# Kernel optimization log

Measured on AMD Instinct MI355X. Metric: run time of the kernel, lower is better.

The kernel has to match this reference:

```python
import jax, jax.numpy as jnp
import numpy as np

B, N, K = 8, 2048, 30  # graphs, points per graph, kNN neighbors


def setup_inputs() -> dict:
    key = jax.random.key(0)
    ks = jax.random.split(key, 16)
    w = lambda k, s: jax.random.normal(k, s, jnp.float32) * 0.05
    z = lambda s: jnp.zeros(s, jnp.float32)
    return {
        "x": jax.random.normal(ks[0], (B * N, 3), jnp.float32),
        "pos": jax.random.normal(ks[1], (B * N, 3), jnp.float32),
        "w1a": w(ks[2], (12, 64)), "b1a": z(64),
        "w1b": w(ks[3], (64, 64)), "b1b": z(64),
        "w2a": w(ks[4], (128, 64)), "b2a": z(64),
        "w2b": w(ks[5], (64, 64)), "b2b": z(64),
        "w3a": w(ks[6], (128, 64)), "b3a": z(64),
        "w3b": w(ks[7], (64, 64)), "b3b": z(64),
        "hw1": w(ks[8], (192, 1024)), "hb1": z(1024),
        "hw2": w(ks[9], (1024, 512)), "hb2": z(512),
        "hw3": w(ks[10], (512, 128)), "hb3": z(128),
        "batch": jnp.repeat(jnp.arange(B, dtype=jnp.int32), N),
        "batch_size": B,
    }


def _knn_idx(f):
    # f: [B,N,d] -> indices of K nearest neighbors (incl. self), [B,N,K]
    d2 = jnp.sum(f * f, axis=-1)  # [B,N]
    dist = d2[:, :, None] + d2[:, None, :] - 2.0 * jnp.einsum('bnd,bmd->bnm', f, f)
    return jax.lax.top_k(-dist, K)[1]


def _edge_conv(f, wa, ba, wb, bb):
    # DynamicEdgeConv: kNN graph on f, message MLP([x_i, x_j - x_i]), max-aggregate
    idx = _knn_idx(f)                                   # [B,N,K]
    xj = jax.vmap(lambda ff, ii: ff[ii])(f, idx)        # [B,N,K,d]
    xi = f[:, :, None, :]
    e = jnp.concatenate([jnp.broadcast_to(xi, xj.shape), xj - xi], axis=-1)
    h = jax.nn.relu(e @ wa + ba)                        # MLP layer 1 (act)
    h = h @ wb + bb                                     # MLP layer 2 (plain last)
    return jnp.max(h, axis=2)                           # max aggr -> [B,N,64]


def reference(x, pos, w1a, b1a, w1b, b1b, w2a, b2a, w2b, b2b, w3a, b3a, w3b, b3b,
              hw1, hb1, hw2, hb2, hw3, hb3, batch, batch_size):
    x0 = jnp.concatenate([x, pos], axis=-1).reshape(batch_size, -1, 6)  # [B,N,6]
    x1 = _edge_conv(x0, w1a, b1a, w1b, b1b)
    x2 = _edge_conv(x1, w2a, b2a, w2b, b2b)
    x3 = _edge_conv(x2, w3a, b3a, w3b, b3b)
    feat = jnp.concatenate([x1, x2, x3], axis=-1)       # [B,N,192]
    h = jax.nn.relu(feat @ hw1 + hb1)                   # head MLP (dropout=eval)
    h = jax.nn.relu(h @ hw2 + hb2)
    out = h @ hw3 + hb3                                 # [B,N,out_channels]
    return out
```

## Files before the change

kernel.cpp:

```cpp
#include <hip/hip_runtime.h>
#include <math.h>

#define BATCH 8
#define NPER 2048
#define NPTS (BATCH*NPER)
#define KNN 30

typedef __attribute__((ext_vector_type(8))) short bf16x8;
typedef __attribute__((ext_vector_type(4))) float f32x4;

__device__ __forceinline__ ushort f2bf(float x) {
    unsigned u = __float_as_uint(x);
    unsigned r = (u + 0x7fffu + ((u >> 16) & 1u)) >> 16;
    return (ushort)r;
}
__device__ __forceinline__ float bf2f(ushort h) {
    return __uint_as_float(((unsigned)h) << 16);
}

__global__ void concat_kernel(const float* __restrict__ x, const float* __restrict__ pos,
                              float* __restrict__ x0) {
    int n = blockIdx.x * blockDim.x + threadIdx.x;
    if (n >= NPTS) return;
#pragma unroll
    for (int d = 0; d < 3; ++d) {
        x0[n*6 + d]     = x[n*3 + d];
        x0[n*6 + 3 + d] = pos[n*3 + d];
    }
}

template<int D>
__global__ void d2_kernel(const float* __restrict__ f, int stride, float* __restrict__ d2) {
    int n = blockIdx.x * blockDim.x + threadIdx.x;
    if (n >= NPTS) return;
    const float* r = f + (size_t)n * stride;
    float s = 0.f;
#pragma unroll
    for (int d = 0; d < D; ++d) s += r[d]*r[d];
    d2[n] = s;
}

template<int D>
__global__ __launch_bounds__(256, 4) void knn4_kernel(const float* __restrict__ f, int stride,
                                                      const float* __restrict__ d2,
                                                      int* __restrict__ idx) {
    __shared__ float sdist[4][NPER];
    __shared__ float sxi[4][(D+3)/4*4];
    __shared__ float sd2n[4];
    int t = threadIdx.x;
    int n0 = blockIdx.x * 4;
    int base = (n0 >> 11) << 11;

    if (t < 4*D) {
        int q = t / D, d = t - q*D;
        sxi[q][d] = f[(size_t)(n0 + q)*stride + d];
    }
    if (t < 4) sd2n[t] = d2[n0 + t];
    __syncthreads();

#pragma unroll 1
    for (int j = 0; j < NPER/256; ++j) {
        int ml = t + 256*j;
        int m = base + ml;
        const float* fm = f + (size_t)m*stride;
        float d2m = d2[m];
        float dot0 = 0.f, dot1 = 0.f, dot2 = 0.f, dot3 = 0.f;
#pragma unroll
        for (int d = 0; d < D; ++d) {
            float a = fm[d];
            dot0 += a*sxi[0][d];
            dot1 += a*sxi[1][d];
            dot2 += a*sxi[2][d];
            dot3 += a*sxi[3][d];
        }
        sdist[0][ml] = sd2n[0] + d2m - 2.f*dot0;
        sdist[1][ml] = sd2n[1] + d2m - 2.f*dot1;
        sdist[2][ml] = sd2n[2] + d2m - 2.f*dot2;
        sdist[3][ml] = sd2n[3] + d2m - 2.f*dot3;
    }
    __syncthreads();

    int w = t >> 6, lane = t & 63;
    int n = n0 + w;

    unsigned u[NPER/64];
#pragma unroll
    for (int i = 0; i < NPER/64; ++i) {
        float dv = sdist[w][lane + 64*i];
        int b = __float_as_int(dv);
        u[i] = (unsigned)(b ^ ((b >> 31) | 0x80000000));
    }

    unsigned T = 0u;
#pragma unroll
    for (int bit = 31; bit >= 0; --bit) {
        unsigned C = T | (1u << bit);
        int c = 0;
#pragma unroll
        for (int i = 0; i < NPER/64; ++i) c += (u[i] < C) ? 1 : 0;
#pragma unroll
        for (int off = 1; off < 64; off <<= 1) c += __shfl_xor(c, off);
        if (c < KNN) T = C;
    }

    unsigned lm = 0u, em = 0u;
#pragma unroll
    for (int i = 0; i < NPER/64; ++i) {
        lm |= (u[i] < T)  ? (1u << i) : 0u;
        em |= (u[i] == T) ? (1u << i) : 0u;
    }
    int nl = __popc(lm);
    int inc = nl;
#pragma unroll
    for (int off = 1; off < 64; off <<= 1) {
        int y = __shfl_up(inc, off);
        if (lane >= off) inc += y;
    }
    int excl = inc - nl;
    int total_less = __shfl(inc, 63);

    int* op = idx + (size_t)n * KNN;
    int slot = excl;
#pragma unroll
    for (int i = 0; i < NPER/64; ++i) {
        if (lm & (1u << i)) { op[slot] = base + i*64 + lane; ++slot; }
    }

    int need = KNN - total_less;
    int running = 0;
#pragma unroll
    for (int i = 0; i < NPER/64; ++i) {
        unsigned long long bal = __ballot((em >> i) & 1u);
        if (bal) {
            unsigned long long lt = bal & ((1ull << lane) - 1ull);
            int r = running + __popcll(lt);
            if (((em >> i) & 1u) && r < need) op[total_less + r] = base + i*64 + lane;
            running += (int)__popcll(bal);
        }
    }
}

__global__ __launch_bounds__(256) void transpose64_kernel(const float* __restrict__ fin, int stride,
                                                          float* __restrict__ fT) {
    __shared__ float tile[64][65];
    int t = threadIdx.x;
    int n0 = blockIdx.x * 64;
#pragma unroll
    for (int i = 0; i < 4; ++i) {
        int id = t + 256*i;
        int r = id >> 4, c4 = (id & 15) * 4;
        float4 v = *reinterpret_cast<const float4*>(&fin[(size_t)(n0 + r)*stride + c4]);
        tile[r][c4] = v.x; tile[r][c4+1] = v.y; tile[r][c4+2] = v.z; tile[r][c4+3] = v.w;
    }
    __syncthreads();
#pragma unroll
    for (int i = 0; i < 16; ++i) {
        int id = t + 256*i;
        int d = id >> 6, nn = id & 63;
        fT[(size_t)d * NPTS + n0 + nn] = tile[nn][d];
    }
}

__global__ __launch_bounds__(256) void knn6_kernel(const float* __restrict__ fq, int qstride,
                                                   const float* __restrict__ fT,
                                                   const float* __restrict__ d2,
                                                   int* __restrict__ idx) {
    __shared__ float sdist[4][NPER];
    __shared__ float sq[4][64];
    __shared__ float sd2n[4];
    int t = threadIdx.x;
    int n0 = blockIdx.x * 4;
    int base = (n0 >> 11) << 11;

    {
        int q = t >> 6, d = t & 63;
        sq[q][d] = fq[(size_t)(n0 + q)*qstride + d];
    }
    if (t < 4) sd2n[t] = d2[n0 + t];
    __syncthreads();

    float acc0[8], acc1[8], acc2[8], acc3[8];
#pragma unroll
    for (int j = 0; j < 8; ++j) { acc0[j] = 0.f; acc1[j] = 0.f; acc2[j] = 0.f; acc3[j] = 0.f; }

    int cbase = base + 8*t;

#pragma unroll 2
    for (int dc = 0; dc < 16; ++dc) {
        int d0 = dc * 4;
        float4 q0 = *reinterpret_cast<const float4*>(&sq[0][d0]);
        float4 q1 = *reinterpret_cast<const float4*>(&sq[1][d0]);
        float4 q2 = *reinterpret_cast<const float4*>(&sq[2][d0]);
        float4 q3 = *reinterpret_cast<const float4*>(&sq[3][d0]);
        float qa0[4] = {q0.x, q0.y, q0.z, q0.w};
        float qa1[4] = {q1.x, q1.y, q1.z, q1.w};
        float qa2[4] = {q2.x, q2.y, q2.z, q2.w};
        float qa3[4] = {q3.x, q3.y, q3.z, q3.w};
#pragma unroll
        for (int dd = 0; dd < 4; ++dd) {
            const float* cp = fT + (size_t)(d0 + dd) * NPTS + cbase;
            float4 c0 = *reinterpret_cast<const float4*>(cp);
            float4 c1 = *reinterpret_cast<const float4*>(cp + 4);
            float cv[8] = {c0.x,c0.y,c0.z,c0.w,c1.x,c1.y,c1.z,c1.w};
#pragma unroll
            for (int j = 0; j < 8; ++j) {
                acc0[j] += cv[j]*qa0[dd];
                acc1[j] += cv[j]*qa1[dd];
                acc2[j] += cv[j]*qa2[dd];
                acc3[j] += cv[j]*qa3[dd];
            }
        }
    }

    {
        float dn0 = sd2n[0], dn1 = sd2n[1], dn2 = sd2n[2], dn3 = sd2n[3];
        float4 dm0 = *reinterpret_cast<const float4*>(&d2[cbase]);
        float4 dm1 = *reinterpret_cast<const float4*>(&d2[cbase + 4]);
        float dmv[8] = {dm0.x,dm0.y,dm0.z,dm0.w,dm1.x,dm1.y,dm1.z,dm1.w};
#pragma unroll
        for (int j = 0; j < 8; ++j) {
            int ml = 8*t + j;
            sdist[0][ml] = dn0 + dmv[j] - 2.f*acc0[j];
            sdist[1][ml] = dn1 + dmv[j] - 2.f*acc1[j];
            sdist[2][ml] = dn2 + dmv[j] - 2.f*acc2[j];
            sdist[3][ml] = dn3 + dmv[j] - 2.f*acc3[j];
        }
    }
    __syncthreads();

    int w = t >> 6, lane = t & 63;
    int n = n0 + w;

    unsigned u[NPER/64];
#pragma unroll
    for (int i = 0; i < NPER/64; ++i) {
        float dv = sdist[w][lane + 64*i];
        int b = __float_as_int(dv);
        u[i] = (unsigned)(b ^ ((b >> 31) | 0x80000000));
    }

    unsigned T = 0u;
#pragma unroll
    for (int bit = 31; bit >= 0; --bit) {
        unsigned C = T | (1u << bit);
        int c = 0;
#pragma unroll
        for (int i = 0; i < NPER/64; ++i) c += (u[i] < C) ? 1 : 0;
#pragma unroll
        for (int off = 1; off < 64; off <<= 1) c += __shfl_xor(c, off);
        if (c < KNN) T = C;
    }

    unsigned lm = 0u, em = 0u;
#pragma unroll
    for (int i = 0; i < NPER/64; ++i) {
        lm |= (u[i] < T)  ? (1u << i) : 0u;
        em |= (u[i] == T) ? (1u << i) : 0u;
    }
    int nl = __popc(lm);
    int inc = nl;
#pragma unroll
    for (int off = 1; off < 64; off <<= 1) {
        int y = __shfl_up(inc, off);
        if (lane >= off) inc += y;
    }
    int excl = inc - nl;
    int total_less = __shfl(inc, 63);

    int* op = idx + (size_t)n * KNN;
    int slot = excl;
#pragma unroll
    for (int i = 0; i < NPER/64; ++i) {
        if (lm & (1u << i)) { op[slot] = base + i*64 + lane; ++slot; }
    }

    int need = KNN - total_less;
    int running = 0;
#pragma unroll
    for (int i = 0; i < NPER/64; ++i) {
        unsigned long long bal = __ballot((em >> i) & 1u);
        if (bal) {
            unsigned long long lt = bal & ((1ull << lane) - 1ull);
            int r = running + __popcll(lt);
            if (((em >> i) & 1u) && r < need) op[total_less + r] = base + i*64 + lane;
            running += (int)__popcll(bal);
        }
    }
}

template<int D>
__global__ __launch_bounds__(256) void gmat_kernel(const float* __restrict__ fin, int in_stride,
                                                   const float* __restrict__ wa,
                                                   float* __restrict__ G) {
    constexpr int DP = (D+3)/4*4;
    __shared__ float sF[64][DP];
    int t = threadIdx.x;
    int row0 = blockIdx.x * 64;
    for (int i = t; i < 64*D; i += 256) {
        int r = i / D, c = i - r*D;
        sF[r][c] = fin[(size_t)(row0 + r)*in_stride + c];
    }
    int w = t >> 6, lane = t & 63;
    float wreg[D];
#pragma unroll
    for (int d = 0; d < D; ++d) wreg[d] = wa[(size_t)(D + d)*64 + lane];
    __syncthreads();
#pragma unroll 1
    for (int pi = 0; pi < 16; ++pi) {
        int p = w*16 + pi;
        float acc = 0.f;
        if constexpr (D % 4 == 0) {
#pragma unroll
            for (int d = 0; d < D; d += 4) {
                float4 fv = *reinterpret_cast<const float4*>(&sF[p][d]);
                acc += fv.x*wreg[d] + fv.y*wreg[d+1] + fv.z*wreg[d+2] + fv.w*wreg[d+3];
            }
        } else {
#pragma unroll
            for (int d = 0; d < D; ++d) acc += sF[p][d]*wreg[d];
        }
        G[(size_t)(row0 + p)*64 + lane] = acc;
    }
}

template<int D>
__global__ __launch_bounds__(256) void edgeconv2_kernel(const float* __restrict__ fin, int in_stride,
                                const float* __restrict__ G,
                                const int* __restrict__ idx,
                                const float* __restrict__ wa, const float* __restrict__ ba,
                                const float* __restrict__ wb, const float* __restrict__ bb,
                                float* __restrict__ fout, int out_stride) {
    __shared__ float sxi[4][(D+3)/4*4];
    __shared__ float sh1[4][2][64];
    int t = threadIdx.x;
    int w = t >> 6, lane = t & 63;
    int n = blockIdx.x * 4 + w;

    float wbc[64];
#pragma unroll
    for (int k = 0; k < 64; ++k) wbc[k] = wb[(size_t)k*64 + lane];
    float bbc = bb[lane];

    if (lane < D) sxi[w][lane] = fin[(size_t)n * in_stride + lane];
    __syncthreads();

    float basec = ba[lane];
#pragma unroll
    for (int d = 0; d < D; ++d)
        basec += sxi[w][d] * (wa[(size_t)d*64 + lane] - wa[(size_t)(D + d)*64 + lane]);

    const int* ip = idx + (size_t)n * KNN;
    int2 jp = *reinterpret_cast<const int2*>(ip);
    float g0 = G[(size_t)jp.x*64 + lane];
    float g1 = G[(size_t)jp.y*64 + lane];
    float maxv = -3.4e38f;
#pragma unroll 1
    for (int jj = 0; jj < KNN; jj += 2) {
        sh1[w][0][lane] = fmaxf(basec + g0, 0.f);
        sh1[w][1][lane] = fmaxf(basec + g1, 0.f);
        int2 jn;
        bool more = (jj + 2 < KNN);
        if (more) jn = *reinterpret_cast<const int2*>(ip + jj + 2);
        __syncthreads();
        if (more) {
            g0 = G[(size_t)jn.x*64 + lane];
            g1 = G[(size_t)jn.y*64 + lane];
        }
        float h20 = bbc, h21 = bbc;
#pragma unroll
        for (int k = 0; k < 64; k += 4) {
            float4 a = *reinterpret_cast<const float4*>(&sh1[w][0][k]);
            float4 b = *reinterpret_cast<const float4*>(&sh1[w][1][k]);
            h20 += a.x*wbc[k] + a.y*wbc[k+1] + a.z*wbc[k+2] + a.w*wbc[k+3];
            h21 += b.x*wbc[k] + b.y*wbc[k+1] + b.z*wbc[k+2] + b.w*wbc[k+3];
        }
        maxv = fmaxf(maxv, fmaxf(h20, h21));
        __syncthreads();
    }
    fout[(size_t)n * out_stride + lane] = maxv;
}

__global__ void wsplit_kernel(const float* __restrict__ w, int K, int N,
                              ushort* __restrict__ hi, ushort* __restrict__ lo, int total) {
    int i = blockIdx.x * 256 + threadIdx.x;
    if (i >= total) return;
    int n = i / K, k = i - n*K;
    float x = w[(size_t)k * N + n];
    ushort h = f2bf(x);
    hi[i] = h;
    lo[i] = f2bf(x - bf2f(h));
}

template<bool RELU>
__global__ __launch_bounds__(256) void mlp_gemm_kernel(
    const float* __restrict__ A, int lda, int K,
    const ushort* __restrict__ Bhi, const ushort* __restrict__ Blo,
    const float* __restrict__ bias, float* __restrict__ C, int N)
{
    __shared__ __align__(16) ushort sAh[64*40];
    __shared__ __align__(16) ushort sAl[64*40];
    __shared__ __align__(16) ushort sBh[64*40];
    __shared__ __align__(16) ushort sBl[64*40];
    int t = threadIdx.x;
    int row0 = blockIdx.x * 64;
    int n0   = blockIdx.y * 64;
    int r = t >> 2, sg = (t & 3) * 8;
    int lane = t & 63, w = t >> 6;
    int wr = w & 1, wc = w >> 1;
    int fr = lane & 15, fk = (lane >> 4) * 8;

    f32x4 acc00 = {0.f,0.f,0.f,0.f}, acc01 = {0.f,0.f,0.f,0.f};
    f32x4 acc10 = {0.f,0.f,0.f,0.f}, acc11 = {0.f,0.f,0.f,0.f};

    const int nk = K / 32;
#pragma unroll 1
    for (int kc = 0; kc < nk; ++kc) {
        int k0 = kc * 32;
        const float* ap = A + (size_t)(row0 + r) * lda + k0 + sg;
        float4 av0 = *reinterpret_cast<const float4*>(ap);
        float4 av1 = *reinterpret_cast<const float4*>(ap + 4);
        float av[8] = {av0.x,av0.y,av0.z,av0.w,av1.x,av1.y,av1.z,av1.w};
        uint ph[4], pl[4];
#pragma unroll
        for (int i = 0; i < 4; ++i) {
            ushort h0 = f2bf(av[2*i]);
            ushort l0 = f2bf(av[2*i]   - bf2f(h0));
            ushort h1 = f2bf(av[2*i+1]);
            ushort l1 = f2bf(av[2*i+1] - bf2f(h1));
            ph[i] = (uint)h0 | ((uint)h1 << 16);
            pl[i] = (uint)l0 | ((uint)l1 << 16);
        }
        uint4 bh = *reinterpret_cast<const uint4*>(Bhi + (size_t)(n0 + r) * K + k0 + sg);
        uint4 bl = *reinterpret_cast<const uint4*>(Blo + (size_t)(n0 + r) * K + k0 + sg);
        __syncthreads();
        *reinterpret_cast<uint4*>(&sAh[r*40 + sg]) = make_uint4(ph[0],ph[1],ph[2],ph[3]);
        *reinterpret_cast<uint4*>(&sAl[r*40 + sg]) = make_uint4(pl[0],pl[1],pl[2],pl[3]);
        *reinterpret_cast<uint4*>(&sBh[r*40 + sg]) = bh;
        *reinterpret_cast<uint4*>(&sBl[r*40 + sg]) = bl;
        __syncthreads();

        bf16x8 a0h = *reinterpret_cast<const bf16x8*>(&sAh[(wr*32 + fr)*40 + fk]);
        bf16x8 a1h = *reinterpret_cast<const bf16x8*>(&sAh[(wr*32 + 16 + fr)*40 + fk]);
        bf16x8 a0l = *reinterpret_cast<const bf16x8*>(&sAl[(wr*32 + fr)*40 + fk]);
        bf16x8 a1l = *reinterpret_cast<const bf16x8*>(&sAl[(wr*32 + 16 + fr)*40 + fk]);
        bf16x8 b0h = *reinterpret_cast<const bf16x8*>(&sBh[(wc*32 + fr)*40 + fk]);
        bf16x8 b1h = *reinterpret_cast<const bf16x8*>(&sBh[(wc*32 + 16 + fr)*40 + fk]);
        bf16x8 b0l = *reinterpret_cast<const bf16x8*>(&sBl[(wc*32 + fr)*40 + fk]);
        bf16x8 b1l = *reinterpret_cast<const bf16x8*>(&sBl[(wc*32 + 16 + fr)*40 + fk]);

        acc00 = __builtin_amdgcn_mfma_f32_16x16x32_bf16(a0h, b0h, acc00, 0, 0, 0);
        acc00 = __builtin_amdgcn_mfma_f32_16x16x32_bf16(a0h, b0l, acc00, 0, 0, 0);
        acc00 = __builtin_amdgcn_mfma_f32_16x16x32_bf16(a0l, b0h, acc00, 0, 0, 0);
        acc01 = __builtin_amdgcn_mfma_f32_16x16x32_bf16(a0h, b1h, acc01, 0, 0, 0);
        acc01 = __builtin_amdgcn_mfma_f32_16x16x32_bf16(a0h, b1l, acc01, 0, 0, 0);
        acc01 = __builtin_amdgcn_mfma_f32_16x16x32_bf16(a0l, b1h, acc01, 0, 0, 0);
        acc10 = __builtin_amdgcn_mfma_f32_16x16x32_bf16(a1h, b0h, acc10, 0, 0, 0);
        acc10 = __builtin_amdgcn_mfma_f32_16x16x32_bf16(a1h, b0l, acc10, 0, 0, 0);
        acc10 = __builtin_amdgcn_mfma_f32_16x16x32_bf16(a1l, b0h, acc10, 0, 0, 0);
        acc11 = __builtin_amdgcn_mfma_f32_16x16x32_bf16(a1h, b1h, acc11, 0, 0, 0);
        acc11 = __builtin_amdgcn_mfma_f32_16x16x32_bf16(a1h, b1l, acc11, 0, 0, 0);
        acc11 = __builtin_amdgcn_mfma_f32_16x16x32_bf16(a1l, b1h, acc11, 0, 0, 0);
    }

    int orow = row0 + wr*32 + (lane >> 4)*4;
    int ocol = n0 + wc*32 + fr;
    float bc0 = bias[ocol];
    float bc1 = bias[ocol + 16];
#pragma unroll
    for (int j = 0; j < 4; ++j) {
        float v00 = acc00[j] + bc0;
        float v01 = acc01[j] + bc1;
        float v10 = acc10[j] + bc0;
        float v11 = acc11[j] + bc1;
        if (RELU) {
            v00 = fmaxf(v00, 0.f); v01 = fmaxf(v01, 0.f);
            v10 = fmaxf(v10, 0.f); v11 = fmaxf(v11, 0.f);
        }
        C[(size_t)(orow + j)*N + ocol]           = v00;
        C[(size_t)(orow + j)*N + ocol + 16]      = v01;
        C[(size_t)(orow + 16 + j)*N + ocol]      = v10;
        C[(size_t)(orow + 16 + j)*N + ocol + 16] = v11;
    }
}

__global__ __launch_bounds__(256) void head_kernel(const float* __restrict__ feat,
                            const float* __restrict__ hw1, const float* __restrict__ hb1,
                            const float* __restrict__ hw2, const float* __restrict__ hb2,
                            const float* __restrict__ hw3, const float* __restrict__ hb3,
                            float* __restrict__ out) {
    __shared__ float smem[16384];
    float* sfeat = smem;
    float* sh1   = smem + 6144;
    int t = threadIdx.x;
    int row0 = blockIdx.x * 32;

    for (int i = t; i < 32*192; i += 256) sfeat[i] = feat[(size_t)row0*192 + i];
    __syncthreads();

    int c4 = t & 127, rh = t >> 7;
    float4 acc2[16];
    {
        float4 b = *reinterpret_cast<const float4*>(&hb2[4*c4]);
#pragma unroll
        for (int i = 0; i < 16; ++i) acc2[i] = b;
    }
    int c1 = t & 63, rg = t >> 6;

    for (int chunk = 0; chunk < 8; ++chunk) {
        int k0 = chunk * 128;
        float acc1a[8], acc1b[8];
        {
            float ba_ = hb1[k0 + c1], bb_ = hb1[k0 + 64 + c1];
#pragma unroll
            for (int i = 0; i < 8; ++i) { acc1a[i] = ba_; acc1b[i] = bb_; }
        }
#pragma unroll 1
        for (int k = 0; k < 192; k += 4) {
            float wA0 = hw1[(size_t)(k+0)*1024 + k0 + c1];
            float wA1 = hw1[(size_t)(k+1)*1024 + k0 + c1];
            float wA2 = hw1[(size_t)(k+2)*1024 + k0 + c1];
            float wA3 = hw1[(size_t)(k+3)*1024 + k0 + c1];
            float wB0 = hw1[(size_t)(k+0)*1024 + k0 + 64 + c1];
            float wB1 = hw1[(size_t)(k+1)*1024 + k0 + 64 + c1];
            float wB2 = hw1[(size_t)(k+2)*1024 + k0 + 64 + c1];
            float wB3 = hw1[(size_t)(k+3)*1024 + k0 + 64 + c1];
#pragma unroll
            for (int i = 0; i < 8; ++i) {
                float4 fv = *reinterpret_cast<const float4*>(&sfeat[(rg + 4*i)*192 + k]);
                acc1a[i] += fv.x*wA0 + fv.y*wA1 + fv.z*wA2 + fv.w*wA3;
                acc1b[i] += fv.x*wB0 + fv.y*wB1 + fv.z*wB2 + fv.w*wB3;
            }
        }
#pragma unroll
        for (int i = 0; i < 8; ++i) {
            sh1[(rg + 4*i)*128 + c1]      = fmaxf(acc1a[i], 0.f);
            sh1[(rg + 4*i)*128 + 64 + c1] = fmaxf(acc1b[i], 0.f);
        }
        __syncthreads();
        float4 wn[4];
#pragma unroll
        for (int q = 0; q < 4; ++q)
            wn[q] = *reinterpret_cast<const float4*>(&hw2[(size_t)(k0 + q)*512 + 4*c4]);
#pragma unroll 1
        for (int k = 0; k < 128; k += 4) {
            float4 wv[4];
#pragma unroll
            for (int q = 0; q < 4; ++q) wv[q] = wn[q];
            if (k + 4 < 128) {
#pragma unroll
                for (int q = 0; q < 4; ++q)
                    wn[q] = *reinterpret_cast<const float4*>(&hw2[(size_t)(k0 + k + 4 + q)*512 + 4*c4]);
            }
#pragma unroll
            for (int i = 0; i < 16; ++i) {
                float4 h4 = *reinterpret_cast<const float4*>(&sh1[(rh + 2*i)*128 + k]);
                acc2[i].x += h4.x*wv[0].x + h4.y*wv[1].x + h4.z*wv[2].x + h4.w*wv[3].x;
                acc2[i].y += h4.x*wv[0].y + h4.y*wv[1].y + h4.z*wv[2].y + h4.w*wv[3].y;
                acc2[i].z += h4.x*wv[0].z + h4.y*wv[1].z + h4.z*wv[2].z + h4.w*wv[3].z;
                acc2[i].w += h4.x*wv[0].w + h4.y*wv[1].w + h4.z*wv[2].w + h4.w*wv[3].w;
            }
        }
        __syncthreads();
    }
#pragma unroll
    for (int i = 0; i < 16; ++i) {
        float4 v;
        v.x = fmaxf(acc2[i].x, 0.f); v.y = fmaxf(acc2[i].y, 0.f);
        v.z = fmaxf(acc2[i].z, 0.f); v.w = fmaxf(acc2[i].w, 0.f);
        *reinterpret_cast<float4*>(&smem[(rh + 2*i)*512 + 4*c4]) = v;
    }
    __syncthreads();
    int c3 = t & 63, rg3 = t >> 6;
    float acc3a[8], acc3b[8];
    {
        float ba_ = hb3[c3], bb_ = hb3[c3 + 64];
#pragma unroll
        for (int i = 0; i < 8; ++i) { acc3a[i] = ba_; acc3b[i] = bb_; }
    }
#pragma unroll 1
    for (int k = 0; k < 512; k += 4) {
        float wA0 = hw3[(size_t)(k+0)*128 + c3];
        float wA1 = hw3[(size_t)(k+1)*128 + c3];
        float wA2 = hw3[(size_t)(k+2)*128 + c3];
        float wA3 = hw3[(size_t)(k+3)*128 + c3];
        float wB0 = hw3[(size_t)(k+0)*128 + c3 + 64];
        float wB1 = hw3[(size_t)(k+1)*128 + c3 + 64];
        float wB2 = hw3[(size_t)(k+2)*128 + c3 + 64];
        float wB3 = hw3[(size_t)(k+3)*128 + c3 + 64];
#pragma unroll
        for (int i = 0; i < 8; ++i) {
            float4 h4 = *reinterpret_cast<const float4*>(&smem[(rg3 + 4*i)*512 + k]);
            acc3a[i] += h4.x*wA0 + h4.y*wA1 + h4.z*wA2 + h4.w*wA3;
            acc3b[i] += h4.x*wB0 + h4.y*wB1 + h4.z*wB2 + h4.w*wB3;
        }
    }
#pragma unroll
    for (int i = 0; i < 8; ++i) {
        out[(size_t)(row0 + rg3 + 4*i)*128 + c3]      = acc3a[i];
        out[(size_t)(row0 + rg3 + 4*i)*128 + c3 + 64] = acc3b[i];
    }
}

extern "C" void kernel_launch(void* const* d_in, const int* in_sizes, int n_in,
                              void* d_out, int out_size, void* d_ws, size_t ws_size,
                              hipStream_t stream) {
    (void)in_sizes; (void)n_in; (void)out_size;
    const float* x   = (const float*)d_in[0];
    const float* pos = (const float*)d_in[1];
    const float* w1a = (const float*)d_in[2];
    const float* b1a = (const float*)d_in[3];
    const float* w1b = (const float*)d_in[4];
    const float* b1b = (const float*)d_in[5];
    const float* w2a = (const float*)d_in[6];
    const float* b2a = (const float*)d_in[7];
    const float* w2b = (const float*)d_in[8];
    const float* b2b = (const float*)d_in[9];
    const float* w3a = (const float*)d_in[10];
    const float* b3a = (const float*)d_in[11];
    const float* w3b = (const float*)d_in[12];
    const float* b3b = (const float*)d_in[13];
    const float* hw1 = (const float*)d_in[14];
    const float* hb1 = (const float*)d_in[15];
    const float* hw2 = (const float*)d_in[16];
    const float* hb2 = (const float*)d_in[17];
    const float* hw3 = (const float*)d_in[18];
    const float* hb3 = (const float*)d_in[19];
    float* out = (float*)d_out;

    float* ws = (float*)d_ws;
    float* x0   = ws;
    float* feat = ws + 98304;
    float* d2b  = ws + 3244032;
    int*   idxb = (int*)(ws + 3260416);
    float* G    = ws + 3751936;
    ushort* w1h = (ushort*)(ws + 4800512);
    ushort* w1l = (ushort*)(ws + 4898816);
    ushort* w2h = (ushort*)(ws + 4997120);
    ushort* w2l = (ushort*)(ws + 5259264);
    ushort* w3h = (ushort*)(ws + 5521408);
    ushort* w3l = (ushort*)(ws + 5554176);
    const size_t base_units = 5586944;

    float* fT = G;

    int ns = 0;
    {
        const int cands[5] = {1, 2, 4, 8, 16};
        for (int ci = 0; ci < 5; ++ci) {
            int c = cands[ci];
            size_t need = (base_units + (size_t)(NPTS / c) * 1536) * 4;
            if (need <= ws_size) { ns = c; break; }
        }
    }

    concat_kernel<<<NPTS/256, 256, 0, stream>>>(x, pos, x0);

    d2_kernel<6><<<NPTS/256, 256, 0, stream>>>(x0, 6, d2b);
    knn4_kernel<6><<<NPTS/4, 256, 0, stream>>>(x0, 6, d2b, idxb);
    gmat_kernel<6><<<NPTS/64, 256, 0, stream>>>(x0, 6, w1a, G);
    edgeconv2_kernel<6><<<NPTS/4, 256, 0, stream>>>(x0, 6, G, idxb, w1a, b1a, w1b, b1b, feat, 192);

    d2_kernel<64><<<NPTS/256, 256, 0, stream>>>(feat, 192, d2b);
    transpose64_kernel<<<NPTS/64, 256, 0, stream>>>(feat, 192, fT);
    knn6_kernel<<<NPTS/4, 256, 0, stream>>>(feat, 192, fT, d2b, idxb);
    gmat_kernel<64><<<NPTS/64, 256, 0, stream>>>(feat, 192, w2a, G);
    edgeconv2_kernel<64><<<NPTS/4, 256, 0, stream>>>(feat, 192, G, idxb, w2a, b2a, w2b, b2b, feat + 64, 192);

    d2_kernel<64><<<NPTS/256, 256, 0, stream>>>(feat + 64, 192, d2b);
    transpose64_kernel<<<NPTS/64, 256, 0, stream>>>(feat + 64, 192, fT);
    knn6_kernel<<<NPTS/4, 256, 0, stream>>>(feat + 64, 192, fT, d2b, idxb);
    gmat_kernel<64><<<NPTS/64, 256, 0, stream>>>(feat + 64, 192, w3a, G);
    edgeconv2_kernel<64><<<NPTS/4, 256, 0, stream>>>(feat + 64, 192, G, idxb, w3a, b3a, w3b, b3b, feat + 128, 192);

    if (ns > 0) {
        wsplit_kernel<<<(192*1024 + 255)/256, 256, 0, stream>>>(hw1, 192, 1024, w1h, w1l, 192*1024);
        wsplit_kernel<<<(1024*512 + 255)/256, 256, 0, stream>>>(hw2, 1024, 512, w2h, w2l, 1024*512);
        wsplit_kernel<<<(512*128 + 255)/256, 256, 0, stream>>>(hw3, 512, 128, w3h, w3l, 512*128);

        int Ms = NPTS / ns;
        float* h1 = ws + base_units;
        float* h2 = h1 + (size_t)Ms * 1024;
        for (int s = 0; s < ns; ++s) {
            const float* As = feat + (size_t)s * Ms * 192;
            float* outs = out + (size_t)s * Ms * 128;
            mlp_gemm_kernel<true ><<<dim3(Ms/64, 1024/64), 256, 0, stream>>>(As, 192, 192, w1h, w1l, hb1, h1, 1024);
            mlp_gemm_kernel<true ><<<dim3(Ms/64,  512/64), 256, 0, stream>>>(h1, 1024, 1024, w2h, w2l, hb2, h2, 512);
            mlp_gemm_kernel<false><<<dim3(Ms/64,  128/64), 256, 0, stream>>>(h2, 512, 512, w3h, w3l, hb3, outs, 128);
        }
    } else {
        head_kernel<<<NPTS/32, 256, 0, stream>>>(feat, hw1, hb1, hw2, hb2, hw3, hb3, out);
    }
}
```

Baseline: 827.1 us.

## Move edge-conv second MLP layer onto split-bf16 MFMA with precomputed base term

Replaces the per-point scalar edge-conv kernel with a new gbase kernel that computes the per-point base term x_i·(Wa_top − Wa_bot) + b, plus an MFMA kernel. The MFMA kernel gathers the 30 neighbor rows for 4 points into shared memory, splits them into bf16 hi/lo pairs, and runs the 64x64 second layer with three bf16 MFMAs per product to keep near-fp32 accuracy. The max reduction is done from the accumulators with cross-lane shuffles. The old kernel's inner FMA loop and per-pair __syncthreads are removed. In exchange it adds weight-split launches, pads each point to 32 rows (2 wasted of 32), and loads B fragments from global memory.

```diff
diff --git a/kernel.cpp b/kernel.cpp
--- a/kernel.cpp
+++ b/kernel.cpp
@@ -324,60 +324,134 @@
 }
 
 template<int D>
-__global__ __launch_bounds__(256) void edgeconv2_kernel(const float* __restrict__ fin, int in_stride,
-                                const float* __restrict__ G,
-                                const int* __restrict__ idx,
-                                const float* __restrict__ wa, const float* __restrict__ ba,
-                                const float* __restrict__ wb, const float* __restrict__ bb,
-                                float* __restrict__ fout, int out_stride) {
-    __shared__ float sxi[4][(D+3)/4*4];
-    __shared__ float sh1[4][2][64];
+__global__ __launch_bounds__(256) void gbase_kernel(const float* __restrict__ fin, int in_stride,
+                                                    const float* __restrict__ wa,
+                                                    const float* __restrict__ ba,
+                                                    float* __restrict__ Gb) {
+    constexpr int DP = (D+7)/8*8;
+    __shared__ float sF[64][DP];
     int t = threadIdx.x;
+    int row0 = blockIdx.x * 64;
+    for (int i = t; i < 64*D; i += 256) {
+        int r = i / D, c = i - r*D;
+        sF[r][c] = fin[(size_t)(row0 + r)*in_stride + c];
+    }
     int w = t >> 6, lane = t & 63;
-    int n = blockIdx.x * 4 + w;
-
-    float wbc[64];
-#pragma unroll
-    for (int k = 0; k < 64; ++k) wbc[k] = wb[(size_t)k*64 + lane];
-    float bbc = bb[lane];
-
-    if (lane < D) sxi[w][lane] = fin[(size_t)n * in_stride + lane];
-    __syncthreads();
-
-    float basec = ba[lane];
+    float wreg[D];
 #pragma unroll
     for (int d = 0; d < D; ++d)
-        basec += sxi[w][d] * (wa[(size_t)d*64 + lane] - wa[(size_t)(D + d)*64 + lane]);
-
-    const int* ip = idx + (size_t)n * KNN;
-    int2 jp = *reinterpret_cast<const int2*>(ip);
-    float g0 = G[(size_t)jp.x*64 + lane];
-    float g1 = G[(size_t)jp.y*64 + lane];
-    float maxv = -3.4e38f;
+        wreg[d] = wa[(size_t)d*64 + lane] - wa[(size_t)(D + d)*64 + lane];
+    float bc = ba[lane];
+    __syncthreads();
 #pragma unroll 1
-    for (int jj = 0; jj < KNN; jj += 2) {
-        sh1[w][0][lane] = fmaxf(basec + g0, 0.f);
-        sh1[w][1][lane] = fmaxf(basec + g1, 0.f);
-        int2 jn;
-        bool more = (jj + 2 < KNN);
-        if (more) jn = *reinterpret_cast<const int2*>(ip + jj + 2);
-        __syncthreads();
-        if (more) {
-            g0 = G[(size_t)jn.x*64 + lane];
-            g1 = G[(size_t)jn.y*64 + lane];
-        }
-        float h20 = bbc, h21 = bbc;
-#pragma unroll
-        for (int k = 0; k < 64; k += 4) {
-            float4 a = *reinterpret_cast<const float4*>(&sh1[w][0][k]);
-            float4 b = *reinterpret_cast<const float4*>(&sh1[w][1][k]);
-            h20 += a.x*wbc[k] + a.y*wbc[k+1] + a.z*wbc[k+2] + a.w*wbc[k+3];
-            h21 += b.x*wbc[k] + b.y*wbc[k+1] + b.z*wbc[k+2] + b.w*wbc[k+3];
-        }
-        maxv = fmaxf(maxv, fmaxf(h20, h21));
-        __syncthreads();
-    }
-    fout[(size_t)n * out_stride + lane] = maxv;
+    for (int pi = 0; pi < 16; ++pi) {
+        int p = w*16 + pi;
+        float acc = bc;
+#pragma unroll
+        for (int d = 0; d < D; ++d) acc += sF[p][d]*wreg[d];
+        Gb[(size_t)(row0 + p)*64 + lane] = acc;
+    }
+}
+
+__global__ __launch_bounds__(256) void edgemfma_kernel(
+    const float* __restrict__ G, const float* __restrict__ Gbase,
+    const int* __restrict__ idx,
+    const ushort* __restrict__ wbTh, const ushort* __restrict__ wbTl,
+    const float* __restrict__ bb,
+    float* __restrict__ fout, int out_stride)
+{
+    __shared__ __align__(16) ushort sHh[128*72];
+    __shared__ __align__(16) ushort sHl[128*72];
+    __shared__ float sbase[4][64];
+    int t = threadIdx.x;
+    int n0 = blockIdx.x * 4;
+
+    {
+        int p = t >> 6, c = t & 63;
+        sbase[p][c] = Gbase[(size_t)(n0 + p)*64 + c];
+    }
+    __syncthreads();
+
+    {
+        int r = t >> 1, c0 = (t & 1) * 32;
+        int p = r >> 5, e = r & 31;
+        int ecl = e < KNN ? e : (KNN - 1);
+        int j = idx[(size_t)(n0 + p)*KNN + ecl];
+        const float* gp = G + (size_t)j*64 + c0;
+        const float* bp = &sbase[p][c0];
+#pragma unroll
+        for (int g = 0; g < 4; ++g) {
+            float4 g0 = *reinterpret_cast<const float4*>(gp + 8*g);
+            float4 g1 = *reinterpret_cast<const float4*>(gp + 8*g + 4);
+            float4 b0 = *reinterpret_cast<const float4*>(bp + 8*g);
+            float4 b1 = *reinterpret_cast<const float4*>(bp + 8*g + 4);
+            float h[8] = {fmaxf(b0.x+g0.x,0.f), fmaxf(b0.y+g0.y,0.f),
+                          fmaxf(b0.z+g0.z,0.f), fmaxf(b0.w+g0.w,0.f),
+                          fmaxf(b1.x+g1.x,0.f), fmaxf(b1.y+g1.y,0.f),
+                          fmaxf(b1.z+g1.z,0.f), fmaxf(b1.w+g1.w,0.f)};
+            uint ph[4], pl[4];
+#pragma unroll
+            for (int i2 = 0; i2 < 4; ++i2) {
+                ushort h0 = f2bf(h[2*i2]);
+                ushort l0 = f2bf(h[2*i2] - bf2f(h0));
+                ushort h1_ = f2bf(h[2*i2+1]);
+                ushort l1 = f2bf(h[2*i2+1] - bf2f(h1_));
+                ph[i2] = (uint)h0 | ((uint)h1_ << 16);
+                pl[i2] = (uint)l0 | ((uint)l1 << 16);
+            }
+            *reinterpret_cast<uint4*>(&sHh[r*72 + c0 + 8*g]) = make_uint4(ph[0],ph[1],ph[2],ph[3]);
+            *reinterpret_cast<uint4*>(&sHl[r*72 + c0 + 8*g]) = make_uint4(pl[0],pl[1],pl[2],pl[3]);
+        }
+    }
+    __syncthreads();
+
+    int lane = t & 63, w = t >> 6;
+    int fr = lane & 15, fk = (lane >> 4) * 8;
+
+    f32x4 acc[2][4];
+#pragma unroll
+    for (int mf = 0; mf < 2; ++mf)
+#pragma unroll
+        for (int nf = 0; nf < 4; ++nf) acc[mf][nf] = f32x4{0.f,0.f,0.f,0.f};
+
+#pragma unroll
+    for (int kk = 0; kk < 2; ++kk) {
+        bf16x8 a0h = *reinterpret_cast<const bf16x8*>(&sHh[(w*32 + fr)*72 + kk*32 + fk]);
+        bf16x8 a1h = *reinterpret_cast<const bf16x8*>(&sHh[(w*32 + 16 + fr)*72 + kk*32 + fk]);
+        bf16x8 a0l = *reinterpret_cast<const bf16x8*>(&sHl[(w*32 + fr)*72 + kk*32 + fk]);
+        bf16x8 a1l = *reinterpret_cast<const bf16x8*>(&sHl[(w*32 + 16 + fr)*72 + kk*32 + fk]);
+#pragma unroll
+        for (int nf = 0; nf < 4; ++nf) {
+            bf16x8 bh = *reinterpret_cast<const bf16x8*>(&wbTh[(size_t)(nf*16 + fr)*64 + kk*32 + fk]);
+            bf16x8 bl = *reinterpret_cast<const bf16x8*>(&wbTl[(size_t)(nf*16 + fr)*64 + kk*32 + fk]);
+            acc[0][nf] = __builtin_amdgcn_mfma_f32_16x16x32_bf16(a0h, bh, acc[0][nf], 0,0,0);
+            acc[0][nf] = __builtin_amdgcn_mfma_f32_16x16x32_bf16(a0h, bl, acc[0][nf], 0,0,0);
+            acc[0][nf] = __builtin_amdgcn_mfma_f32_16x16x32_bf16(a0l, bh, acc[0][nf], 0,0,0);
+            acc[1][nf] = __builtin_amdgcn_mfma_f32_16x16x32_bf16(a1h, bh, acc[1][nf], 0,0,0);
+            acc[1][nf] = __builtin_amdgcn_mfma_f32_16x16x32_bf16(a1h, bl, acc[1][nf], 0,0,0);
+            acc[1][nf] = __builtin_amdgcn_mfma_f32_16x16x32_bf16(a1l, bh, acc[1][nf], 0,0,0);
+        }
+    }
+
+#pragma unroll
+    for (int nf = 0; nf < 4; ++nf) {
+        float vmax = -3.4e38f;
+#pragma unroll
+        for (int mf = 0; mf < 2; ++mf) {
+#pragma unroll
+            for (int j = 0; j < 4; ++j) {
+                int lr = mf*16 + ((lane >> 4) << 2) + j;
+                float v = acc[mf][nf][j];
+                vmax = (lr < KNN) ? fmaxf(vmax, v) : vmax;
+            }
+        }
+        vmax = fmaxf(vmax, __shfl_xor(vmax, 16));
+        vmax = fmaxf(vmax, __shfl_xor(vmax, 32));
+        if (lane < 16) {
+            int c = nf*16 + lane;
+            fout[(size_t)(n0 + w)*out_stride + c] = vmax + bb[c];
+        }
+    }
 }
 
 __global__ void wsplit_kernel(const float* __restrict__ w, int K, int N,
@@ -639,7 +713,14 @@
     ushort* w2l = (ushort*)(ws + 5259264);
     ushort* w3h = (ushort*)(ws + 5521408);
     ushort* w3l = (ushort*)(ws + 5554176);
-    const size_t base_units = 5586944;
+    ushort* wb1h = (ushort*)(ws + 5586944);
+    ushort* wb1l = (ushort*)(ws + 5588992);
+    ushort* wb2h = (ushort*)(ws + 5591040);
+    ushort* wb2l = (ushort*)(ws + 5593088);
+    ushort* wb3h = (ushort*)(ws + 5595136);
+    ushort* wb3l = (ushort*)(ws + 5597184);
+    float* Gbase = ws + 5599232;
+    const size_t base_units = 6647808;
 
     float* fT = G;
 
@@ -653,30 +734,36 @@
         }
     }
 
+    wsplit_kernel<<<(192*1024 + 255)/256, 256, 0, stream>>>(hw1, 192, 1024, w1h, w1l, 192*1024);
+    wsplit_kernel<<<(1024*512 + 255)/256, 256, 0, stream>>>(hw2, 1024, 512, w2h, w2l, 1024*512);
+    wsplit_kernel<<<(512*128 + 255)/256, 256, 0, stream>>>(hw3, 512, 128, w3h, w3l, 512*128);
+    wsplit_kernel<<<16, 256, 0, stream>>>(w1b, 64, 64, wb1h, wb1l, 4096);
+    wsplit_kernel<<<16, 256, 0, stream>>>(w2b, 64, 64, wb2h, wb2l, 4096);
+    wsplit_kernel<<<16, 256, 0, stream>>>(w3b, 64, 64, wb3h, wb3l, 4096);
+
     concat_kernel<<<NPTS/256, 256, 0, stream>>>(x, pos, x0);
 
     d2_kernel<6><<<NPTS/256, 256, 0, stream>>>(x0, 6, d2b);
     knn4_kernel<6><<<NPTS/4, 256, 0, stream>>>(x0, 6, d2b, idxb);
     gmat_kernel<6><<<NPTS/64, 256, 0, stream>>>(x0, 6, w1a, G);
-    edgeconv2_kernel<6><<<NPTS/4, 256, 0, stream>>>(x0, 6, G, idxb, w1a, b1a, w1b, b1b, feat, 192);
+    gbase_kernel<6><<<NPTS/64, 256, 0, stream>>>(x0, 6, w1a, b1a, Gbase);
+    edgemfma_kernel<<<NPTS/4, 256, 0, stream>>>(G, Gbase, idxb, wb1h, wb1l, b1b, feat, 192);
 
     d2_kernel<64><<<NPTS/256, 256, 0, stream>>>(feat, 192, d2b);
     transpose64_kernel<<<NPTS/64, 256, 0, stream>>>(feat, 192, fT);
     knn6_kernel<<<NPTS/4, 256, 0, stream>>>(feat, 192, fT, d2b, idxb);
     gmat_kernel<64><<<NPTS/64, 256, 0, stream>>>(feat, 192, w2a, G);
-    edgeconv2_kernel<64><<<NPTS/4, 256, 0, stream>>>(feat, 192, G, idxb, w2a, b2a, w2b, b2b, feat + 64, 192);
+    gbase_kernel<64><<<NPTS/64, 256, 0, stream>>>(feat, 192, w2a, b2a, Gbase);
+    edgemfma_kernel<<<NPTS/4, 256, 0, stream>>>(G, Gbase, idxb, wb2h, wb2l, b2b, feat + 64, 192);
 
     d2_kernel<64><<<NPTS/256, 256, 0, stream>>>(feat + 64, 192, d2b);
     transpose64_kernel<<<NPTS/64, 256, 0, stream>>>(feat + 64, 192, fT);
     knn6_kernel<<<NPTS/4, 256, 0, stream>>>(feat + 64, 192, fT, d2b, idxb);
     gmat_kernel<64><<<NPTS/64, 256, 0, stream>>>(feat + 64, 192, w3a, G);
-    edgeconv2_kernel<64><<<NPTS/4, 256, 0, stream>>>(feat + 64, 192, G, idxb, w3a, b3a, w3b, b3b, feat + 128, 192);
+    gbase_kernel<64><<<NPTS/64, 256, 0, stream>>>(feat + 64, 192, w3a, b3a, Gbase);
+    edgemfma_kernel<<<NPTS/4, 256, 0, stream>>>(G, Gbase, idxb, wb3h, wb3l, b3b, feat + 128, 192);
 
     if (ns > 0) {
-        wsplit_kernel<<<(192*1024 + 255)/256, 256, 0, stream>>>(hw1, 192, 1024, w1h, w1l, 192*1024);
-        wsplit_kernel<<<(1024*512 + 255)/256, 256, 0, stream>>>(hw2, 1024, 512, w2h, w2l, 1024*512);
-        wsplit_kernel<<<(512*128 + 255)/256, 256, 0, stream>>>(hw3, 512, 128, w3h, w3l, 512*128);
-
         int Ms = NPTS / ns;
         float* h1 = ws + base_units;
         float* h2 = h1 + (size_t)Ms * 1024;
```

Result: faster. 744.6 us (-10.0%).
